# Kernel optimization log

Hardware: AMD Instinct MI355X
Metric: run time of the kernel (lower is better)

The kernel has to match this reference:

```python
import jax, jax.numpy as jnp
import numpy as np

SENSOR_H, SENSOR_W = 256, 256
SPP = 16
BATCH, C, H_IMG, W_IMG = 4, 3, 1024, 1024


def setup_inputs() -> dict:
    key = jax.random.key(0)
    k1, k2 = jax.random.split(key)
    img = jax.random.uniform(k1, (BATCH, C, H_IMG, W_IMG), dtype=jnp.float32)
    jitter = jax.random.uniform(k2, (SPP, SENSOR_H, SENSOR_W, 2), dtype=jnp.float32)
    t = jnp.ones((1,), jnp.float32)
    return {"img": img, "t": t, "jitter": jitter}


def deform(pos, t):
    # Analytic per-axis foveation diffeomorphism [-1,1]^2 -> [-1,1]^2:
    #   f(u) = tanh(t*u)/tanh(t), f'(u) = t*(1 - tanh(t*u)^2)/tanh(t)
    # Jacobian is diagonal, so det = f'(x) * f'(y).
    tt = t[0]
    s = jnp.tanh(tt)
    th = jnp.tanh(tt * pos)
    warped = th / s                      # (..., 2)
    dd = tt * (1.0 - th * th) / s        # diagonal Jacobian entries (..., 2)
    det = dd[..., 0] * dd[..., 1]        # (...)
    return warped, det


def grid_sample_border(img, grid):
    # img: (b,c,H,W); grid: (spp,h,w,2) in [-1,1]
    # bilinear, padding_mode='border', align_corners=False (matches F.grid_sample)
    b, c, H, W = img.shape
    gx = (grid[..., 0] + 1.0) * (W / 2.0) - 0.5
    gy = (grid[..., 1] + 1.0) * (H / 2.0) - 0.5
    gx = jnp.clip(gx, 0.0, W - 1.0)
    gy = jnp.clip(gy, 0.0, H - 1.0)
    x0 = jnp.floor(gx)
    y0 = jnp.floor(gy)
    wx = (gx - x0)[None, None]           # (1,1,spp,h,w)
    wy = (gy - y0)[None, None]
    x0i = jnp.clip(x0.astype(jnp.int32), 0, W - 1)
    y0i = jnp.clip(y0.astype(jnp.int32), 0, H - 1)
    x1i = jnp.clip(x0i + 1, 0, W - 1)
    y1i = jnp.clip(y0i + 1, 0, H - 1)
    # fancy-index gather: result (b,c,spp,h,w); avoids tiling img over (b*spp)
    v00 = img[:, :, y0i, x0i]
    v01 = img[:, :, y0i, x1i]
    v10 = img[:, :, y1i, x0i]
    v11 = img[:, :, y1i, x1i]
    return (v00 * (1 - wx) * (1 - wy) + v01 * wx * (1 - wy)
            + v10 * (1 - wx) * wy + v11 * wx * wy)


def reference(img, t, jitter):
    step_x = 2.0 / SENSOR_W
    step_y = 2.0 / SENSOR_H
    px = jnp.arange(-1.0, 1.0, step_x, dtype=jnp.float32)
    py = jnp.arange(-1.0, 1.0, step_y, dtype=jnp.float32)
    gx, gy = jnp.meshgrid(px, py, indexing='xy')          # (h, w)
    pixel_pos = jnp.stack((gx, gy), axis=-1)[None]        # (1, h, w, 2)
    jit = jitter * jnp.array([step_x, step_y], jnp.float32)
    pos = pixel_pos + jit                                 # (spp, h, w, 2)
    warped, det = deform(pos, t)                          # (spp,h,w,2), (spp,h,w)
    samples = grid_sample_border(img, warped)             # (b, c, spp, h, w)
    weighted = jnp.mean(samples * det[None, None], axis=2)  # (b, c, h, w)
    area = jnp.mean(det, axis=0)[None, None]              # (1, 1, h, w)
    return weighted / area
```

## Files before the change

kernel.cpp:

```cpp
#include <hip/hip_runtime.h>
#include <hip/hip_fp16.h>

#define SPP   16
#define SH    256
#define SW    256
#define HI    1024
#define WI    1024
#define CH    3
#define BATCH 4

#define TS    16
#define MAXD  88
#define NTHR  512

__device__ __forceinline__ float fast_tanh(float x) {
    const float e = __expf(2.0f * x);
    return (e - 1.0f) * __builtin_amdgcn_rcpf(e + 1.0f);
}

__global__ __launch_bounds__(NTHR, 6) void foveated_tile(
    const float* __restrict__ img,
    const float* __restrict__ t_ptr,
    const float* __restrict__ jitter,
    float* __restrict__ out)
{
    __shared__ __half2 lds_rg[MAXD * MAXD];
    __shared__ __half  lds_b [MAXD * MAXD];

    const int bid  = blockIdx.x;
    const int L    = (bid & 7) * 128 + (bid >> 3);
    const int b    = L >> 8;
    const int trow = (L >> 4) & 15;
    const int tcol = L & 15;
    const int sx0  = tcol * TS;
    const int sy0  = trow * TS;

    const float step  = 2.0f / 256.0f;
    const float tt    = t_ptr[0];
    const float inv_s = __builtin_amdgcn_rcpf(fast_tanh(tt));

    auto gmap = [&](float p) {
        float g = (fast_tanh(tt * p) * inv_s + 1.0f) * 512.0f - 0.5f;
        return fminf(fmaxf(g, 0.0f), 1023.0f);
    };
    const float pxmin = -1.0f + sx0 * step, pxmax = pxmin + TS * step;
    const float pymin = -1.0f + sy0 * step, pymax = pymin + TS * step;
    const int x_lo = max((int)gmap(pxmin) - 1, 0);
    const int x_hi = min((int)gmap(pxmax) + 2, WI - 1);
    const int y_lo = max((int)gmap(pymin) - 1, 0);
    const int y_hi = min((int)gmap(pymax) + 2, HI - 1);
    const int ncols = x_hi - x_lo + 1;
    const int nrows = y_hi - y_lo + 1;
    const bool fits = (ncols <= MAXD) && (nrows <= MAXD);

    const size_t plane = (size_t)HI * WI;
    const float* __restrict__ p0 = img + (size_t)(b * CH) * plane;
    const float* __restrict__ p1 = p0 + plane;
    const float* __restrict__ p2 = p1 + plane;

    const int th = threadIdx.x;
    const int h  = th & 1;
    const int p  = th >> 1;
    const int sx = sx0 + (p & 15);
    const int sy = sy0 + (p >> 4);

    const float px = -1.0f + sx * step;
    const float py = -1.0f + sy * step;

    float acc0 = 0.0f, acc1 = 0.0f, acc2 = 0.0f, dsum = 0.0f;

    const float2* __restrict__ jit2 = (const float2*)jitter;
    const int jbase = h * 8 * (SH * SW) + sy * SW + sx;

    if (fits) {
        const int npix = nrows * ncols;
        const unsigned mdiv = (1u << 22) / (unsigned)ncols + 1u;
        for (int i = th; i < npix; i += NTHR) {
            const int r = (int)(((unsigned)i * mdiv) >> 22);
            const int c = i - r * ncols;
            const int g = (y_lo + r) * WI + (x_lo + c);
            lds_rg[r * MAXD + c] = __floats2half2_rn(p0[g], p1[g]);
            lds_b [r * MAXD + c] = __float2half_rn(p2[g]);
        }
        __syncthreads();

        #pragma unroll 2
        for (int k = 0; k < 8; ++k) {
            const float2 j = jit2[k * (SH * SW) + jbase];
            const float posx = px + j.x * step;
            const float posy = py + j.y * step;

            const float thx = fast_tanh(tt * posx);
            const float thy = fast_tanh(tt * posy);
            const float ddx = tt * (1.0f - thx * thx) * inv_s;
            const float ddy = tt * (1.0f - thy * thy) * inv_s;
            const float det = ddx * ddy;

            float gx = (thx * inv_s + 1.0f) * 512.0f - 0.5f;
            float gy = (thy * inv_s + 1.0f) * 512.0f - 0.5f;
            gx = fminf(fmaxf(gx, 0.0f), (float)(WI - 1));
            gy = fminf(fmaxf(gy, 0.0f), (float)(HI - 1));

            const int xb = min((int)gx, WI - 2);
            const int yb = min((int)gy, HI - 2);
            const float fx = gx - (float)xb;
            const float fy = gy - (float)yb;

            const float w00 = (1.0f - fx) * (1.0f - fy) * det;
            const float w01 = fx * (1.0f - fy) * det;
            const float w10 = (1.0f - fx) * fy * det;
            const float w11 = fx * fy * det;
            dsum += det;

            const int lidx = (yb - y_lo) * MAXD + (xb - x_lo);
            const float2 f00 = __half22float2(lds_rg[lidx]);
            const float2 f01 = __half22float2(lds_rg[lidx + 1]);
            const float2 f10 = __half22float2(lds_rg[lidx + MAXD]);
            const float2 f11 = __half22float2(lds_rg[lidx + MAXD + 1]);
            const float v00 = __half2float(lds_b[lidx]);
            const float v01 = __half2float(lds_b[lidx + 1]);
            const float v10 = __half2float(lds_b[lidx + MAXD]);
            const float v11 = __half2float(lds_b[lidx + MAXD + 1]);

            acc0 += w00 * f00.x + w01 * f01.x + w10 * f10.x + w11 * f11.x;
            acc1 += w00 * f00.y + w01 * f01.y + w10 * f10.y + w11 * f11.y;
            acc2 += w00 * v00   + w01 * v01   + w10 * v10   + w11 * v11;
        }
    } else {
        #pragma unroll 2
        for (int k = 0; k < 8; ++k) {
            const float2 j = jit2[k * (SH * SW) + jbase];
            const float posx = px + j.x * step;
            const float posy = py + j.y * step;

            const float thx = fast_tanh(tt * posx);
            const float thy = fast_tanh(tt * posy);
            const float ddx = tt * (1.0f - thx * thx) * inv_s;
            const float ddy = tt * (1.0f - thy * thy) * inv_s;
            const float det = ddx * ddy;

            float gx = (thx * inv_s + 1.0f) * 512.0f - 0.5f;
            float gy = (thy * inv_s + 1.0f) * 512.0f - 0.5f;
            gx = fminf(fmaxf(gx, 0.0f), (float)(WI - 1));
            gy = fminf(fmaxf(gy, 0.0f), (float)(HI - 1));

            const int xb = min((int)gx, WI - 2);
            const int yb = min((int)gy, HI - 2);
            const float fx = gx - (float)xb;
            const float fy = gy - (float)yb;

            const float w00 = (1.0f - fx) * (1.0f - fy) * det;
            const float w01 = fx * (1.0f - fy) * det;
            const float w10 = (1.0f - fx) * fy * det;
            const float w11 = fx * fy * det;
            dsum += det;

            const int i0 = yb * WI + xb;
            const int i1 = i0 + WI;
            { const float2 a = *(const float2*)(p0 + i0), c2 = *(const float2*)(p0 + i1);
              acc0 += a.x * w00 + a.y * w01 + c2.x * w10 + c2.y * w11; }
            { const float2 a = *(const float2*)(p1 + i0), c2 = *(const float2*)(p1 + i1);
              acc1 += a.x * w00 + a.y * w01 + c2.x * w10 + c2.y * w11; }
            { const float2 a = *(const float2*)(p2 + i0), c2 = *(const float2*)(p2 + i1);
              acc2 += a.x * w00 + a.y * w01 + c2.x * w10 + c2.y * w11; }
        }
    }

    acc0 += __shfl_xor(acc0, 1);
    acc1 += __shfl_xor(acc1, 1);
    acc2 += __shfl_xor(acc2, 1);
    dsum += __shfl_xor(dsum, 1);

    if (h == 0) {
        const float inv_d = 1.0f / dsum;
        const int pix = sy * SW + sx;
        const size_t ob = (size_t)b * CH * (SH * SW) + pix;
        out[ob]                 = acc0 * inv_d;
        out[ob + (SH * SW)]     = acc1 * inv_d;
        out[ob + 2 * (SH * SW)] = acc2 * inv_d;
    }
}

extern "C" void kernel_launch(void* const* d_in, const int* in_sizes, int n_in,
                              void* d_out, int out_size, void* d_ws, size_t ws_size,
                              hipStream_t stream) {
    const float* img    = (const float*)d_in[0];
    const float* t      = (const float*)d_in[1];
    const float* jitter = (const float*)d_in[2];
    float* out          = (float*)d_out;

    hipLaunchKernelGGL(foveated_tile, dim3(1024), dim3(NTHR), 0, stream,
                       img, t, jitter, out);
}
```

Measured before the change: 108.1 us.

## Shrink sensor tiles to 8x8 with padded LDS stride and prefetched jitter

Cuts the sensor tile from 16x16 to 8x8 pixels with 128-thread blocks and four times as many blocks, so each block stages a smaller image footprint (up to 48x48) in LDS. The LDS row stride is padded to 49 to reduce bank conflicts. All eight jitter samples are loaded into registers before the LDS fill, overlapping those loads with staging. The fallback path uses scalar loads instead of float2 loads, which also avoids misaligned vector accesses. Smaller tiles mean more halo overhead per pixel and more blocks to schedule.

```diff
diff --git a/kernel.cpp b/kernel.cpp
--- a/kernel.cpp
+++ b/kernel.cpp
@@ -9,29 +9,30 @@
 #define CH    3
 #define BATCH 4
 
-#define TS    16
-#define MAXD  88
-#define NTHR  512
+#define TS    8
+#define MAXD  48
+#define LSTR  49
+#define NTHR  128
 
 __device__ __forceinline__ float fast_tanh(float x) {
     const float e = __expf(2.0f * x);
     return (e - 1.0f) * __builtin_amdgcn_rcpf(e + 1.0f);
 }
 
-__global__ __launch_bounds__(NTHR, 6) void foveated_tile(
+__global__ __launch_bounds__(NTHR, 6) void foveated_tile8(
     const float* __restrict__ img,
     const float* __restrict__ t_ptr,
     const float* __restrict__ jitter,
     float* __restrict__ out)
 {
-    __shared__ __half2 lds_rg[MAXD * MAXD];
-    __shared__ __half  lds_b [MAXD * MAXD];
+    __shared__ __half2 lds_rg[MAXD * LSTR];
+    __shared__ __half  lds_b [MAXD * LSTR];
 
     const int bid  = blockIdx.x;
-    const int L    = (bid & 7) * 128 + (bid >> 3);
-    const int b    = L >> 8;
-    const int trow = (L >> 4) & 15;
-    const int tcol = L & 15;
+    const int L    = (bid & 7) * 512 + (bid >> 3);
+    const int b    = L >> 10;
+    const int trow = (L >> 5) & 31;
+    const int tcol = L & 31;
     const int sx0  = tcol * TS;
     const int sy0  = trow * TS;
 
@@ -61,16 +62,19 @@
     const int th = threadIdx.x;
     const int h  = th & 1;
     const int p  = th >> 1;
-    const int sx = sx0 + (p & 15);
-    const int sy = sy0 + (p >> 4);
+    const int sx = sx0 + (p & 7);
+    const int sy = sy0 + (p >> 3);
 
     const float px = -1.0f + sx * step;
     const float py = -1.0f + sy * step;
 
-    float acc0 = 0.0f, acc1 = 0.0f, acc2 = 0.0f, dsum = 0.0f;
-
     const float2* __restrict__ jit2 = (const float2*)jitter;
     const int jbase = h * 8 * (SH * SW) + sy * SW + sx;
+    float2 jv[8];
+    #pragma unroll
+    for (int k = 0; k < 8; ++k) jv[k] = jit2[k * (SH * SW) + jbase];
+
+    float acc0 = 0.0f, acc1 = 0.0f, acc2 = 0.0f, dsum = 0.0f;
 
     if (fits) {
         const int npix = nrows * ncols;
@@ -79,16 +83,15 @@
             const int r = (int)(((unsigned)i * mdiv) >> 22);
             const int c = i - r * ncols;
             const int g = (y_lo + r) * WI + (x_lo + c);
-            lds_rg[r * MAXD + c] = __floats2half2_rn(p0[g], p1[g]);
-            lds_b [r * MAXD + c] = __float2half_rn(p2[g]);
+            lds_rg[r * LSTR + c] = __floats2half2_rn(p0[g], p1[g]);
+            lds_b [r * LSTR + c] = __float2half_rn(p2[g]);
         }
         __syncthreads();
 
         #pragma unroll 2
         for (int k = 0; k < 8; ++k) {
-            const float2 j = jit2[k * (SH * SW) + jbase];
-            const float posx = px + j.x * step;
-            const float posy = py + j.y * step;
+            const float posx = px + jv[k].x * step;
+            const float posy = py + jv[k].y * step;
 
             const float thx = fast_tanh(tt * posx);
             const float thy = fast_tanh(tt * posy);
@@ -112,15 +115,15 @@
             const float w11 = fx * fy * det;
             dsum += det;
 
-            const int lidx = (yb - y_lo) * MAXD + (xb - x_lo);
+            const int lidx = (yb - y_lo) * LSTR + (xb - x_lo);
             const float2 f00 = __half22float2(lds_rg[lidx]);
             const float2 f01 = __half22float2(lds_rg[lidx + 1]);
-            const float2 f10 = __half22float2(lds_rg[lidx + MAXD]);
-            const float2 f11 = __half22float2(lds_rg[lidx + MAXD + 1]);
+            const float2 f10 = __half22float2(lds_rg[lidx + LSTR]);
+            const float2 f11 = __half22float2(lds_rg[lidx + LSTR + 1]);
             const float v00 = __half2float(lds_b[lidx]);
             const float v01 = __half2float(lds_b[lidx + 1]);
-            const float v10 = __half2float(lds_b[lidx + MAXD]);
-            const float v11 = __half2float(lds_b[lidx + MAXD + 1]);
+            const float v10 = __half2float(lds_b[lidx + LSTR]);
+            const float v11 = __half2float(lds_b[lidx + LSTR + 1]);
 
             acc0 += w00 * f00.x + w01 * f01.x + w10 * f10.x + w11 * f11.x;
             acc1 += w00 * f00.y + w01 * f01.y + w10 * f10.y + w11 * f11.y;
@@ -129,9 +132,8 @@
     } else {
         #pragma unroll 2
         for (int k = 0; k < 8; ++k) {
-            const float2 j = jit2[k * (SH * SW) + jbase];
-            const float posx = px + j.x * step;
-            const float posy = py + j.y * step;
+            const float posx = px + jv[k].x * step;
+            const float posy = py + jv[k].y * step;
 
             const float thx = fast_tanh(tt * posx);
             const float thy = fast_tanh(tt * posy);
@@ -157,12 +159,12 @@
 
             const int i0 = yb * WI + xb;
             const int i1 = i0 + WI;
-            { const float2 a = *(const float2*)(p0 + i0), c2 = *(const float2*)(p0 + i1);
-              acc0 += a.x * w00 + a.y * w01 + c2.x * w10 + c2.y * w11; }
-            { const float2 a = *(const float2*)(p1 + i0), c2 = *(const float2*)(p1 + i1);
-              acc1 += a.x * w00 + a.y * w01 + c2.x * w10 + c2.y * w11; }
-            { const float2 a = *(const float2*)(p2 + i0), c2 = *(const float2*)(p2 + i1);
-              acc2 += a.x * w00 + a.y * w01 + c2.x * w10 + c2.y * w11; }
+            { const float a0 = p0[i0], a1 = p0[i0 + 1], c0 = p0[i1], c1 = p0[i1 + 1];
+              acc0 += a0 * w00 + a1 * w01 + c0 * w10 + c1 * w11; }
+            { const float a0 = p1[i0], a1 = p1[i0 + 1], c0 = p1[i1], c1 = p1[i1 + 1];
+              acc1 += a0 * w00 + a1 * w01 + c0 * w10 + c1 * w11; }
+            { const float a0 = p2[i0], a1 = p2[i0 + 1], c0 = p2[i1], c1 = p2[i1 + 1];
+              acc2 += a0 * w00 + a1 * w01 + c0 * w10 + c1 * w11; }
         }
     }
 
@@ -189,6 +191,6 @@
     const float* jitter = (const float*)d_in[2];
     float* out          = (float*)d_out;
 
-    hipLaunchKernelGGL(foveated_tile, dim3(1024), dim3(NTHR), 0, stream,
+    hipLaunchKernelGGL(foveated_tile8, dim3(4096), dim3(NTHR), 0, stream,
                        img, t, jitter, out);
 }
```

Result: slower. 125.1 us (+15.7%).
